# Kernel optimization log

Hardware: AMD Instinct MI355X
Metric: run time of the kernel (lower is better)

The kernel has to match this reference:

```python
import jax, jax.numpy as jnp
import numpy as np

FORGET_BIAS = 1.0  # TF BasicLSTMCell default

B, T, D, H = 64, 1024, 300, 512


def setup_inputs() -> dict:
    key = jax.random.key(0)
    k1, k2, k3 = jax.random.split(key, 3)
    essays = jax.random.normal(k1, (B, T, D), dtype=jnp.float32)
    # TF BasicLSTMCell: single kernel [D+H, 4H], gate order (i, j, f, o)
    W_lstm = jax.random.normal(k2, (D + H, 4 * H), dtype=jnp.float32) * 0.05
    b_lstm = jnp.zeros((4 * H,), dtype=jnp.float32)
    W_dense = jax.random.normal(k3, (H, 1), dtype=jnp.float32) * 0.05
    b_dense = jnp.zeros((1,), dtype=jnp.float32)
    return {"essays": essays, "W_lstm": W_lstm, "b_lstm": b_lstm,
            "W_dense": W_dense, "b_dense": b_dense}


def _lstm_scan(essays, W_lstm, b_lstm):
    # Precompute input projection for all timesteps: [B,T,4H]
    Wx, Wh = W_lstm[:D], W_lstm[D:]
    x_proj = jnp.einsum('btd,dg->btg', essays, Wx) + b_lstm

    def step(carry, xp):
        c, h = carry
        gates = xp + h @ Wh  # [B,4H]
        i, j, f, o = jnp.split(gates, 4, axis=-1)
        new_c = c * jax.nn.sigmoid(f + FORGET_BIAS) + jax.nn.sigmoid(i) * jnp.tanh(j)
        new_h = jnp.tanh(new_c) * jax.nn.sigmoid(o)
        return (new_c, new_h), new_h

    init = (jnp.zeros((essays.shape[0], H), essays.dtype),
            jnp.zeros((essays.shape[0], H), essays.dtype))
    _, hs = jax.lax.scan(step, init, jnp.swapaxes(x_proj, 0, 1))  # hs: [T,B,H]
    return jnp.swapaxes(hs, 0, 1)  # [B,T,H]


def reference(essays, W_lstm, b_lstm, W_dense, b_dense):
    lstm_out = _lstm_scan(essays, W_lstm, b_lstm)      # [B,T,H]
    mot = jnp.mean(lstm_out, axis=1)                   # mean-over-time pooling [B,H]
    preds = jax.nn.sigmoid(mot @ W_dense + b_dense)    # [B,1]
    return preds.reshape(-1)                           # [B]
```

## Files before the change

### kernel.cpp

```cpp
#include <hip/hip_runtime.h>
#include <hip/hip_bf16.h>
#include <stdint.h>

#define B_   64
#define T_   1024
#define D_   300
#define H_   512
#define G4H  2048
#define KP   320

typedef __attribute__((ext_vector_type(8))) short short8;
typedef __attribute__((ext_vector_type(4))) float f32x4;
typedef unsigned long long ull;

__device__ __forceinline__ unsigned short f2bf(float v) {
    __hip_bfloat16 h = __float2bfloat16(v);
    return *reinterpret_cast<unsigned short*>(&h);
}
__device__ __forceinline__ float bf2f(unsigned u) {
    return __uint_as_float(u << 16);
}
__device__ __forceinline__ float sigm(float x) { return 1.f / (1.f + __expf(-x)); }
__device__ __forceinline__ float tanhfast(float x) {
    float e = __expf(2.f * x);
    return 1.f - 2.f / (e + 1.f);
}

__device__ __forceinline__ void bar_lds() {
    asm volatile("s_waitcnt lgkmcnt(0)" ::: "memory");
    __builtin_amdgcn_s_barrier();
    asm volatile("" ::: "memory");
}

#define ASYNC16(g, l)                                                        \
    __builtin_amdgcn_global_load_lds(                                        \
        (const __attribute__((address_space(1))) void*)(g),                  \
        (__attribute__((address_space(3))) void*)(l), 16, 0, 0)

__global__ void cvt_essays(const float* __restrict__ es, unsigned short* __restrict__ Ab) {
    unsigned i = blockIdx.x * 256u + threadIdx.x;
    unsigned row = i / KP;
    unsigned col = i - row * KP;
    float v = (col < D_) ? es[(size_t)row * D_ + col] : 0.f;
    Ab[i] = f2bf(v);
}

__global__ void cvt_misc(const float* __restrict__ Wl, unsigned short* __restrict__ Bt) {
    unsigned i = blockIdx.x * 256u + threadIdx.x;
    unsigned n = i / KP, k = i - n * KP;
    float v = (k < D_) ? Wl[(size_t)k * G4H + n] : 0.f;
    Bt[i] = f2bf(v);
}

__global__ void cvt_wh(const float* __restrict__ Wl, unsigned short* __restrict__ WhTg) {
    unsigned i = blockIdx.x * 256u + threadIdx.x;
    unsigned gc = i & 2047u, k = i >> 11;
    WhTg[(size_t)gc * 512 + k] = f2bf(Wl[(size_t)(300 + k) * G4H + gc]);
}

__global__ void poison_hfp(unsigned* __restrict__ hfp) {
    hfp[blockIdx.x * 256u + threadIdx.x] = 0xAAAAAAAAu;
}

__global__ __launch_bounds__(256) void gemm_xp(
    const unsigned short* __restrict__ Ab,
    const unsigned short* __restrict__ Bt,
    const float* __restrict__ bias,
    unsigned short* __restrict__ xpr)
{
    __shared__ __align__(16) unsigned short Al[128 * 32];
    __shared__ __align__(16) unsigned short Bl[128 * 32];
    const int tid = threadIdx.x;
    const int w = tid >> 6, lane = tid & 63;
    const int ln = lane & 15, q = lane >> 4;
    const int bx = blockIdx.x;
    const int m0 = (bx >> 4) * 128;
    const int n0 = (bx & 15) * 128;
    const int wr = w >> 1, wc = w & 1;

    f32x4 acc[4][4];
#pragma unroll
    for (int i = 0; i < 4; i++)
#pragma unroll
        for (int j = 0; j < 4; j++) acc[i][j] = (f32x4){0.f, 0.f, 0.f, 0.f};

    for (int k0 = 0; k0 < KP; k0 += 32) {
#pragma unroll
        for (int it = 0; it < 2; ++it) {
            int s = it * 4 + w;
            int c = s * 64 + lane;
            int r = c >> 2;
            int ko = (c & 3) * 8;
            ASYNC16(Ab + (size_t)(m0 + r) * KP + k0 + ko, &Al[s * 512]);
            ASYNC16(Bt + (size_t)(n0 + r) * KP + k0 + ko, &Bl[s * 512]);
        }
        __syncthreads();
        short8 af[4], bf[4];
#pragma unroll
        for (int mt = 0; mt < 4; ++mt)
            af[mt] = *(const short8*)&Al[(wr * 64 + mt * 16 + ln) * 32 + q * 8];
#pragma unroll
        for (int nt = 0; nt < 4; ++nt)
            bf[nt] = *(const short8*)&Bl[(wc * 64 + nt * 16 + ln) * 32 + q * 8];
#pragma unroll
        for (int mt = 0; mt < 4; ++mt)
#pragma unroll
            for (int nt = 0; nt < 4; ++nt)
                acc[mt][nt] = __builtin_amdgcn_mfma_f32_16x16x32_bf16(af[mt], bf[nt], acc[mt][nt], 0, 0, 0);
        __syncthreads();
    }
#pragma unroll
    for (int mt = 0; mt < 4; ++mt) {
#pragma unroll
        for (int nt = 0; nt < 4; ++nt) {
            int col = n0 + wc * 64 + nt * 16 + ln;
            int gate = col >> 9, r9 = col & 511;
            int slice = r9 >> 4, jj = r9 & 15;
            float bb = bias[col];
#pragma unroll
            for (int r = 0; r < 4; ++r) {
                int row = m0 + wr * 64 + mt * 16 + q * 4 + r;
                int t = row & 1023, bglob = row >> 10;
                int g = bglob >> 4, bloc = bglob & 15;
                size_t idx = ((((size_t)t * 4 + g) * 32 + slice) * 16 + bloc) * 64
                             + gate * 16 + jj;
                xpr[idx] = f2bf(acc[mt][nt][r] + bb);
            }
        }
    }
}

__global__ __launch_bounds__(256, 1) void lstm_rec(
    const unsigned short* __restrict__ WhTg,
    const unsigned short* __restrict__ xpr,
    unsigned* __restrict__ hfp,
    float* __restrict__ hmean)
{
    __shared__ __align__(16) unsigned short WhT[64 * 520];
    __shared__ __align__(16) unsigned short hl[16 * 520];
    __shared__ float gbuf[4][16][17];

    const int tid = threadIdx.x;
    const int bid = blockIdx.x;
    const int g     = bid >> 5;
    const int slice = bid & 31;
    const int j0    = slice * 16;
    const int bg    = g * 16;
    const int wv = tid >> 6, lane = tid & 63, ln = lane & 15, q = lane >> 4;
    const bool skip = (tid >= 8 * slice) && (tid < 8 * slice + 8);

    for (int ch = tid; ch < 64 * 64; ch += 256) {
        int c = ch >> 6, off = (ch & 63) * 8;
        int gc = (c >> 4) * 512 + j0 + (c & 15);
        *(uint4*)&WhT[c * 520 + off] = *(const uint4*)&WhTg[(size_t)gc * 512 + off];
    }

    const int b = tid >> 4;
    const int j = tid & 15;
    const int rowoff = (bg + b) * 512;

    {
        ull* hl8 = (ull*)hl;
#pragma unroll
        for (int i = 0; i < 16; ++i) {
            int c = tid + (i << 8);
            int row = c >> 8, pair = c & 255;
            hl8[(row * 1040 + pair * 8) >> 3] = 0ull;
        }
    }
    __syncthreads();

    float c_st = 0.f, hsum = 0.f;
    const unsigned short* xblk0 = xpr + ((size_t)g * 32 + slice) * 1024 + b * 64 + j;
    unsigned short xc0 = xblk0[0], xc1 = xblk0[16], xc2 = xblk0[32], xc3 = xblk0[48];
    unsigned short xn0 = xc0, xn1 = xc1, xn2 = xc2, xn3 = xc3;

    for (int t = 0; t < T_; ++t) {
        if (t + 1 < T_) {
            const unsigned short* xr = xblk0 + (size_t)(t + 1) * 131072;
            xn0 = xr[0]; xn1 = xr[16]; xn2 = xr[32]; xn3 = xr[48];
        }
        if (t > 0 && !skip) {
            const ull* src = (const ull*)(hfp + (size_t)(t & 1) * 32768 + bg * 512);
            const unsigned want = (unsigned)((t >> 1) & 3);
            ull v[16];
#pragma unroll
            for (int i = 0; i < 16; ++i)
                v[i] = __hip_atomic_load(src + tid + (i << 8),
                                         __ATOMIC_RELAXED, __HIP_MEMORY_SCOPE_AGENT);
            while (true) {
                unsigned bad = 0u;
#pragma unroll
                for (int i = 0; i < 16; ++i) {
                    unsigned lo = (unsigned)v[i], hi = (unsigned)(v[i] >> 32);
                    bad |= ((((lo & 3u) ^ want) | ((hi & 3u) ^ want)) != 0u) ? (1u << i) : 0u;
                }
                if (!bad) break;
#pragma unroll
                for (int i = 0; i < 16; ++i)
                    if (bad & (1u << i))
                        v[i] = __hip_atomic_load(src + tid + (i << 8),
                                                 __ATOMIC_RELAXED, __HIP_MEMORY_SCOPE_AGENT);
            }
#pragma unroll
            for (int i = 0; i < 16; ++i) {
                int c = tid + (i << 8);
                int row = c >> 8, pair = c & 255;
                unsigned u = (unsigned)f2bf(__uint_as_float((unsigned)v[i]))
                           | ((unsigned)f2bf(__uint_as_float((unsigned)(v[i] >> 32))) << 16);
                *(unsigned*)((char*)hl + row * 1040 + pair * 4) = u;
            }
        }
        bar_lds();

        f32x4 acc = (f32x4){0.f, 0.f, 0.f, 0.f};
#pragma unroll
        for (int kk = 0; kk < 16; ++kk) {
            short8 av = *(const short8*)&hl[ln * 520 + kk * 32 + q * 8];
            short8 bv = *(const short8*)&WhT[(wv * 16 + ln) * 520 + kk * 32 + q * 8];
            acc = __builtin_amdgcn_mfma_f32_16x16x32_bf16(av, bv, acc, 0, 0, 0);
        }
#pragma unroll
        for (int r = 0; r < 4; ++r)
            gbuf[wv][q * 4 + r][ln] = acc[r];
        bar_lds();

        float ai  = gbuf[0][b][j] + bf2f((unsigned)xc0);
        float aj  = gbuf[1][b][j] + bf2f((unsigned)xc1);
        float af_ = gbuf[2][b][j] + bf2f((unsigned)xc2);
        float ao  = gbuf[3][b][j] + bf2f((unsigned)xc3);
        float si = sigm(ai), tj = tanhfast(aj);
        float sf = sigm(af_ + 1.0f), so = sigm(ao);
        c_st = c_st * sf + si * tj;
        float h = tanhfast(c_st) * so;
        hsum += h;
        xc0 = xn0; xc1 = xn1; xc2 = xn2; xc3 = xn3;

        hl[b * 520 + j0 + j] = f2bf(h);

        unsigned hb = (__float_as_uint(h) & ~3u) | (unsigned)(((t + 1) >> 1) & 3);
        __hip_atomic_store(hfp + (size_t)((t + 1) & 1) * 32768 + rowoff + j0 + j,
                           hb, __ATOMIC_RELAXED, __HIP_MEMORY_SCOPE_AGENT);
    }
    hmean[(size_t)rowoff + j0 + j] = hsum * (1.f / 1024.f);
}

__global__ void dense_out(const float* __restrict__ hmean, const float* __restrict__ Wd,
                          const float* __restrict__ bd, float* __restrict__ out) {
    int bb = blockIdx.x;
    int lane = threadIdx.x;
    float p = 0.f;
    for (int e = lane; e < H_; e += 64) p += hmean[(size_t)bb * H_ + e] * Wd[e];
#pragma unroll
    for (int off = 32; off; off >>= 1) p += __shfl_down(p, off);
    if (lane == 0) out[bb] = 1.f / (1.f + __expf(-(p + bd[0])));
}

extern "C" void kernel_launch(void* const* d_in, const int* in_sizes, int n_in,
                              void* d_out, int out_size, void* d_ws, size_t ws_size,
                              hipStream_t stream) {
    const float* essays  = (const float*)d_in[0];
    const float* W_lstm  = (const float*)d_in[1];
    const float* b_lstm  = (const float*)d_in[2];
    const float* W_dense = (const float*)d_in[3];
    const float* b_dense = (const float*)d_in[4];
    float* out = (float*)d_out;

    char* ws = (char*)d_ws;
    unsigned short* xp   = (unsigned short*)(ws);
    unsigned short* Ab   = (unsigned short*)(ws + 268435456ull);
    unsigned short* Bt   = (unsigned short*)(ws + 310378496ull);
    unsigned short* WhTg = (unsigned short*)(ws + 311689216ull);
    unsigned*       hfp  = (unsigned*)(ws + 268435456ull);
    float*          hm   = (float*)(ws + 268435456ull + 262144ull);

    hipLaunchKernelGGL(cvt_essays, dim3(81920), dim3(256), 0, stream, essays, Ab);
    hipLaunchKernelGGL(cvt_misc,   dim3(2560),  dim3(256), 0, stream, W_lstm, Bt);
    hipLaunchKernelGGL(cvt_wh,     dim3(4096),  dim3(256), 0, stream, W_lstm, WhTg);
    hipLaunchKernelGGL(gemm_xp,    dim3(8192),  dim3(256), 0, stream, Ab, Bt, b_lstm, xp);
    hipLaunchKernelGGL(poison_hfp, dim3(256),   dim3(256), 0, stream, hfp);
    hipLaunchKernelGGL(lstm_rec,   dim3(128),   dim3(256), 0, stream, WhTg, xp, hfp, hm);
    hipLaunchKernelGGL(dense_out,  dim3(64),    dim3(64),  0, stream, hm, W_dense, b_dense, out);
}
```

Baseline: 3.593 ms.

## Replace tag-bit polling on hidden state with per-wave step counter flags

The recurrent kernel used to embed a 2-bit epoch tag in the low bits of every stored hidden value and spin on all 16 loaded words until every tag matched. Now each wave writes its h values, waits for its stores to complete, and then publishes a per-wave step counter. Consumers poll four counter words before loading the hidden state once. This cuts the polling traffic and stops h being truncated by the tag bits. In exchange it adds a store fence and a flag round trip on the critical path, and it relies on relaxed atomics being ordered correctly.

```diff
diff --git a/kernel.cpp b/kernel.cpp
--- a/kernel.cpp
+++ b/kernel.cpp
@@ -58,8 +58,8 @@
     WhTg[(size_t)gc * 512 + k] = f2bf(Wl[(size_t)(300 + k) * G4H + gc]);
 }
 
-__global__ void poison_hfp(unsigned* __restrict__ hfp) {
-    hfp[blockIdx.x * 256u + threadIdx.x] = 0xAAAAAAAAu;
+__global__ void init_hfp(unsigned* __restrict__ hfp) {
+    hfp[blockIdx.x * 256u + threadIdx.x] = 0u;
 }
 
 __global__ __launch_bounds__(256) void gemm_xp(
@@ -134,6 +134,7 @@
     const unsigned short* __restrict__ WhTg,
     const unsigned short* __restrict__ xpr,
     unsigned* __restrict__ hfp,
+    unsigned* __restrict__ flags,
     float* __restrict__ hmean)
 {
     __shared__ __align__(16) unsigned short WhT[64 * 520];
@@ -147,7 +148,7 @@
     const int j0    = slice * 16;
     const int bg    = g * 16;
     const int wv = tid >> 6, lane = tid & 63, ln = lane & 15, q = lane >> 4;
-    const bool skip = (tid >= 8 * slice) && (tid < 8 * slice + 8);
+    const bool skip = (tid >> 3) == slice;
 
     for (int ch = tid; ch < 64 * 64; ch += 256) {
         int c = ch >> 6, off = (ch & 63) * 8;
@@ -175,33 +176,27 @@
     unsigned short xc0 = xblk0[0], xc1 = xblk0[16], xc2 = xblk0[32], xc3 = xblk0[48];
     unsigned short xn0 = xc0, xn1 = xc1, xn2 = xc2, xn3 = xc3;
 
+    const ull* fp = (const ull*)(flags + (g * 32 + (tid >> 3)) * 4);
+
     for (int t = 0; t < T_; ++t) {
         if (t + 1 < T_) {
             const unsigned short* xr = xblk0 + (size_t)(t + 1) * 131072;
             xn0 = xr[0]; xn1 = xr[16]; xn2 = xr[32]; xn3 = xr[48];
         }
         if (t > 0 && !skip) {
+            const unsigned wantf = (unsigned)t;
+            while (true) {
+                ull f01 = __hip_atomic_load(fp,     __ATOMIC_RELAXED, __HIP_MEMORY_SCOPE_AGENT);
+                ull f23 = __hip_atomic_load(fp + 1, __ATOMIC_RELAXED, __HIP_MEMORY_SCOPE_AGENT);
+                if ((unsigned)f01 >= wantf && (unsigned)(f01 >> 32) >= wantf &&
+                    (unsigned)f23 >= wantf && (unsigned)(f23 >> 32) >= wantf) break;
+            }
             const ull* src = (const ull*)(hfp + (size_t)(t & 1) * 32768 + bg * 512);
-            const unsigned want = (unsigned)((t >> 1) & 3);
             ull v[16];
 #pragma unroll
             for (int i = 0; i < 16; ++i)
                 v[i] = __hip_atomic_load(src + tid + (i << 8),
                                          __ATOMIC_RELAXED, __HIP_MEMORY_SCOPE_AGENT);
-            while (true) {
-                unsigned bad = 0u;
-#pragma unroll
-                for (int i = 0; i < 16; ++i) {
-                    unsigned lo = (unsigned)v[i], hi = (unsigned)(v[i] >> 32);
-                    bad |= ((((lo & 3u) ^ want) | ((hi & 3u) ^ want)) != 0u) ? (1u << i) : 0u;
-                }
-                if (!bad) break;
-#pragma unroll
-                for (int i = 0; i < 16; ++i)
-                    if (bad & (1u << i))
-                        v[i] = __hip_atomic_load(src + tid + (i << 8),
-                                                 __ATOMIC_RELAXED, __HIP_MEMORY_SCOPE_AGENT);
-            }
 #pragma unroll
             for (int i = 0; i < 16; ++i) {
                 int c = tid + (i << 8);
@@ -238,9 +233,12 @@
 
         hl[b * 520 + j0 + j] = f2bf(h);
 
-        unsigned hb = (__float_as_uint(h) & ~3u) | (unsigned)(((t + 1) >> 1) & 3);
         __hip_atomic_store(hfp + (size_t)((t + 1) & 1) * 32768 + rowoff + j0 + j,
-                           hb, __ATOMIC_RELAXED, __HIP_MEMORY_SCOPE_AGENT);
+                           __float_as_uint(h), __ATOMIC_RELAXED, __HIP_MEMORY_SCOPE_AGENT);
+        asm volatile("s_waitcnt vmcnt(0)" ::: "memory");
+        if ((tid & 63) == 0)
+            __hip_atomic_store(flags + (g * 32 + slice) * 4 + wv, (unsigned)(t + 1),
+                               __ATOMIC_RELAXED, __HIP_MEMORY_SCOPE_AGENT);
     }
     hmean[(size_t)rowoff + j0 + j] = hsum * (1.f / 1024.f);
 }
@@ -272,13 +270,14 @@
     unsigned short* Bt   = (unsigned short*)(ws + 310378496ull);
     unsigned short* WhTg = (unsigned short*)(ws + 311689216ull);
     unsigned*       hfp  = (unsigned*)(ws + 268435456ull);
-    float*          hm   = (float*)(ws + 268435456ull + 262144ull);
+    unsigned*       flg  = (unsigned*)(ws + 268435456ull + 262144ull);
+    float*          hm   = (float*)(ws + 268435456ull + 264192ull);
 
     hipLaunchKernelGGL(cvt_essays, dim3(81920), dim3(256), 0, stream, essays, Ab);
     hipLaunchKernelGGL(cvt_misc,   dim3(2560),  dim3(256), 0, stream, W_lstm, Bt);
     hipLaunchKernelGGL(cvt_wh,     dim3(4096),  dim3(256), 0, stream, W_lstm, WhTg);
     hipLaunchKernelGGL(gemm_xp,    dim3(8192),  dim3(256), 0, stream, Ab, Bt, b_lstm, xp);
-    hipLaunchKernelGGL(poison_hfp, dim3(256),   dim3(256), 0, stream, hfp);
-    hipLaunchKernelGGL(lstm_rec,   dim3(128),   dim3(256), 0, stream, WhTg, xp, hfp, hm);
+    hipLaunchKernelGGL(init_hfp,   dim3(258),   dim3(256), 0, stream, hfp);
+    hipLaunchKernelGGL(lstm_rec,   dim3(128),   dim3(256), 0, stream, WhTg, xp, hfp, flg, hm);
     hipLaunchKernelGGL(dense_out,  dim3(64),    dim3(64),  0, stream, hm, W_dense, b_dense, out);
 }
```

Result: slower. 5.008 ms (+39.4%).
